# Performance work log

Hardware: AMD Instinct MI355X
Metric: run time of the kernel (lower is better)

## Reference

```python
import jax, jax.numpy as jnp
import numpy as np

B, S, D = 4, 2048, 1024
NH, NKV = 16, 4
DK = D // NH          # 64
NG = NH // NKV        # 4


def _rope_tables(seq, d_k):
    theta = 1.0 / jnp.power(10000.0, jnp.arange(0, d_k, 2, dtype=jnp.float32) / d_k)
    ang = jnp.outer(jnp.arange(seq, dtype=jnp.float32), theta)  # [S, DK/2]
    ang = jnp.concatenate([ang, ang], axis=-1)                   # [S, DK]
    return jnp.cos(ang), jnp.sin(ang)


def _rotate_half(t):
    half = t.shape[-1] // 2
    return jnp.concatenate([-t[..., half:], t[..., :half]], axis=-1)


def _apply_rope(t, cos, sin):
    # t: [B, H, S, DK]; cos/sin: [S, DK]
    return t * cos + _rotate_half(t) * sin


def setup_inputs() -> dict:
    key = jax.random.key(0)
    ks = jax.random.split(key, 5)
    sc = 0.02
    x = jax.random.normal(ks[0], (B, S, D), dtype=jnp.float32)
    Wq = jax.random.normal(ks[1], (D, NH * DK), dtype=jnp.float32) * sc
    Wk = jax.random.normal(ks[2], (D, NKV * DK), dtype=jnp.float32) * sc
    Wv = jax.random.normal(ks[3], (D, NKV * DK), dtype=jnp.float32) * sc
    Wo = jax.random.normal(ks[4], (D, D), dtype=jnp.float32) * sc
    mask = jnp.tril(jnp.ones((S, S), dtype=bool))[None, None]  # causal [1,1,S,S]
    return {"x": x, "Wq": Wq, "Wk": Wk, "Wv": Wv, "Wo": Wo, "mask": mask}


def reference(x, Wq, Wk, Wv, Wo, mask):
    batch, seq, _ = x.shape
    q = (x @ Wq).reshape(batch, seq, NH, DK).transpose(0, 2, 1, 3)    # [B,NH,S,DK]
    k = (x @ Wk).reshape(batch, seq, NKV, DK).transpose(0, 2, 1, 3)   # [B,NKV,S,DK]
    v = (x @ Wv).reshape(batch, seq, NKV, DK).transpose(0, 2, 1, 3)

    cos, sin = _rope_tables(seq, DK)
    q = _apply_rope(q, cos, sin)
    k = _apply_rope(k, cos, sin)

    # GQA: repeat_interleave K/V along head dim
    k = jnp.repeat(k, NG, axis=1)  # [B,NH,S,DK]
    v = jnp.repeat(v, NG, axis=1)

    scores = jnp.einsum('bhqd,bhkd->bhqk', q, k) / jnp.sqrt(jnp.float32(DK))
    scores = jnp.where(mask, scores, jnp.float32(-jnp.inf))
    weights = jax.nn.softmax(scores, axis=-1)
    out = jnp.einsum('bhqk,bhkd->bhqd', weights, v)          # [B,NH,S,DK]
    out = out.transpose(0, 2, 1, 3).reshape(batch, seq, D)   # [B,S,D]
    return out @ Wo
```

## Files before the change

### kernel.cpp

```cpp
#include <hip/hip_runtime.h>

#define DEV __device__ __forceinline__

typedef short s16x8 __attribute__((ext_vector_type(8)));
typedef float f32x4 __attribute__((ext_vector_type(4)));


DEV unsigned short f2bf(float f) {
  union { float f; unsigned int u; } a; a.f = f;
  unsigned int u = a.u;
  u = (u + 0x7FFFu + ((u >> 16) & 1u)) >> 16;
  return (unsigned short)u;
}

DEV unsigned int bfpack2(float a, float b) {
  union { float f; unsigned int u; } x, y; x.f = a; y.f = b;
  return ((x.u + 0x8000u) >> 16) | ((y.u + 0x8000u) & 0xFFFF0000u);
}

DEV unsigned int pktrunc(float a, float b) {
  union { float f; unsigned int u; } x, y; x.f = a; y.f = b;
  return __builtin_amdgcn_perm(y.u, x.u, 0x07060302u);
}

DEV void gl_lds16(const void* g, void* l) {
  __builtin_amdgcn_global_load_lds(
      (const __attribute__((address_space(1))) unsigned int*)g,
      (__attribute__((address_space(3))) unsigned int*)l, 16, 0, 0);
}

__global__ __launch_bounds__(256) void cvt_kern(const float* __restrict__ src,
                                                unsigned short* __restrict__ dst) {
  int i = blockIdx.x * 256 + threadIdx.x;
  float4 v = ((const float4*)src)[i];
  ushort4 o = make_ushort4(f2bf(v.x), f2bf(v.y), f2bf(v.z), f2bf(v.w));
  ((ushort4*)dst)[i] = o;
}

__global__ __launch_bounds__(256) void transp_kern(const float* __restrict__ src,
                                                   unsigned short* __restrict__ dst,
                                                   int src_cols, int dst_off) {
  __shared__ float tile[32][33];
  int k0 = blockIdx.x * 32, n0 = blockIdx.y * 32;
  int tx = threadIdx.x & 31, ty = threadIdx.x >> 5;
  #pragma unroll
  for (int i = ty; i < 32; i += 8)
    tile[i][tx] = src[(k0 + i) * src_cols + (n0 + tx)];
  __syncthreads();
  #pragma unroll
  for (int i = ty; i < 32; i += 8)
    dst[(size_t)(n0 + i + dst_off) * 1024 + (k0 + tx)] = f2bf(tile[tx][i]);
}

__global__ __launch_bounds__(256) void transp_qkv(const float* __restrict__ Wq,
                                                  const float* __restrict__ Wk,
                                                  const float* __restrict__ Wv,
                                                  unsigned short* __restrict__ dst) {
  __shared__ float tile[32][33];
  int k0 = blockIdx.x * 32, n0 = blockIdx.y * 32;
  const float* src; int sc, nloc;
  if (n0 < 1024)      { src = Wq; sc = 1024; nloc = n0; }
  else if (n0 < 1280) { src = Wk; sc = 256;  nloc = n0 - 1024; }
  else                { src = Wv; sc = 256;  nloc = n0 - 1280; }
  int tx = threadIdx.x & 31, ty = threadIdx.x >> 5;
  #pragma unroll
  for (int i = ty; i < 32; i += 8)
    tile[i][tx] = src[(k0 + i) * sc + (nloc + tx)];
  __syncthreads();
  #pragma unroll
  for (int i = ty; i < 32; i += 8)
    dst[(size_t)(n0 + i) * 1024 + (k0 + tx)] = f2bf(tile[tx][i]);
}

template <int EPI>
__global__ __launch_bounds__(256) void gemm128(
    const unsigned short* __restrict__ A,
    const unsigned short* __restrict__ BT,
    unsigned short* __restrict__ Qbuf,
    unsigned short* __restrict__ Kbuf,
    unsigned short* __restrict__ VTbuf,
    float* __restrict__ Cout) {
  __shared__ __align__(16) unsigned short As[128 * 64];
  __shared__ __align__(16) unsigned short Bs[128 * 64];
  const int K = 1024;
  int m0 = blockIdx.x * 128, n0 = blockIdx.y * 128;
  int tid = threadIdx.x, w = tid >> 6, lane = tid & 63;
  int c4 = lane & 15, quad = lane >> 4;
  int x7 = c4 & 7;
  int m_off = (w & 1) * 64, n_off = (w >> 1) * 64;

  f32x4 acc[4][4];
  #pragma unroll
  for (int i = 0; i < 4; i++)
    #pragma unroll
    for (int j = 0; j < 4; j++) acc[i][j] = (f32x4){0.f, 0.f, 0.f, 0.f};

  const unsigned short* pA[4];
  const unsigned short* pB[4];
  #pragma unroll
  for (int i = 0; i < 4; ++i) {
    int slot = i * 256 + tid;
    int row = slot >> 3, cs = slot & 7, lc = cs ^ (row & 7);
    pA[i] = A + (size_t)(m0 + row) * K + lc * 8;
    pB[i] = BT + (size_t)(n0 + row) * K + lc * 8;
  }

  for (int kt = 0; kt < K / 64; ++kt) {
    __syncthreads();
    #pragma unroll
    for (int i = 0; i < 4; ++i) {
      int slot = i * 256 + tid;
      gl_lds16(pA[i], (char*)As + slot * 16);
      gl_lds16(pB[i], (char*)Bs + slot * 16);
      pA[i] += 64; pB[i] += 64;
    }
    __syncthreads();
    #pragma unroll
    for (int kk = 0; kk < 2; ++kk) {
      s16x8 a[4], b[4];
      int cc = ((kk * 4 + quad) ^ x7) * 16;
      #pragma unroll
      for (int mi = 0; mi < 4; ++mi)
        a[mi] = *(const s16x8*)((const char*)As + (m_off + mi * 16 + c4) * 128 + cc);
      #pragma unroll
      for (int ni = 0; ni < 4; ++ni)
        b[ni] = *(const s16x8*)((const char*)Bs + (n_off + ni * 16 + c4) * 128 + cc);
      #pragma unroll
      for (int mi = 0; mi < 4; ++mi)
        #pragma unroll
        for (int ni = 0; ni < 4; ++ni)
          acc[mi][ni] = __builtin_amdgcn_mfma_f32_16x16x32_bf16(a[mi], b[ni], acc[mi][ni], 0, 0, 0);
    }
  }

  if (EPI == 1) {
    #pragma unroll
    for (int mi = 0; mi < 4; ++mi)
      #pragma unroll
      for (int ni = 0; ni < 4; ++ni)
        #pragma unroll
        for (int r = 0; r < 4; ++r) {
          int row = m0 + m_off + mi * 16 + quad * 4 + r;
          int col = n0 + n_off + ni * 16 + c4;
          Cout[(size_t)row * 1024 + col] = acc[mi][ni][r];
        }
  } else {
    int colbase = n0 + n_off;
    if (colbase < 1280) {
      const float CTH = 0.41524101186092029f;
      const float SC = 0.18033688011112042f;
      float th0 = exp2f(-(float)c4 * CTH);
      float th1 = exp2f(-(float)(c4 + 16) * CTH);
      bool isQ = colbase < 1024;
      float osc = isQ ? SC : 1.0f;
      #pragma unroll
      for (int mi = 0; mi < 4; ++mi)
        #pragma unroll
        for (int r = 0; r < 4; ++r) {
          int row = m0 + m_off + mi * 16 + quad * 4 + r;
          float pos = (float)(row & 2047);
          float a0 = pos * th0, a1 = pos * th1;
          float c0 = __cosf(a0), s0 = __sinf(a0);
          float c1 = __cosf(a1), s1 = __sinf(a1);
          float v0 = acc[mi][0][r], v1 = acc[mi][1][r];
          float v2 = acc[mi][2][r], v3 = acc[mi][3][r];
          float o0 = (v0 * c0 - v2 * s0) * osc;
          float o1 = (v1 * c1 - v3 * s1) * osc;
          float o2 = (v2 * c0 + v0 * s0) * osc;
          float o3 = (v3 * c1 + v1 * s1) * osc;
          if (isQ) {
            size_t base = (size_t)row * 1024 + colbase + c4;
            Qbuf[base] = f2bf(o0); Qbuf[base + 16] = f2bf(o1);
            Qbuf[base + 32] = f2bf(o2); Qbuf[base + 48] = f2bf(o3);
          } else {
            size_t base = (size_t)row * 256 + (colbase - 1024) + c4;
            Kbuf[base] = f2bf(o0); Kbuf[base + 16] = f2bf(o1);
            Kbuf[base + 32] = f2bf(o2); Kbuf[base + 48] = f2bf(o3);
          }
        }
    } else {
      #pragma unroll
      for (int mi = 0; mi < 4; ++mi)
        #pragma unroll
        for (int ni = 0; ni < 4; ++ni) {
          int row = m0 + m_off + mi * 16 + quad * 4;
          int c = colbase + ni * 16 + c4 - 1280;
          int bb = row >> 11, s = row & 2047;
          uint2 pv = make_uint2(bfpack2(acc[mi][ni][0], acc[mi][ni][1]),
                                bfpack2(acc[mi][ni][2], acc[mi][ni][3]));
          *(uint2*)(VTbuf + ((size_t)(bb * 256 + c)) * 2048 + s) = pv;
        }
    }
  }
}

__global__ __launch_bounds__(128, 2) void attn_kern(
    const unsigned short* __restrict__ Qbuf,
    const unsigned short* __restrict__ Kbuf,
    const unsigned short* __restrict__ VTbuf,
    unsigned short* __restrict__ Obuf) {
  __shared__ __align__(16) unsigned short Ks[2][64 * 64];
  __shared__ __align__(16) unsigned short VTs[2][64 * 64];
  __shared__ __align__(16) unsigned short Ps[2 * 32 * 64];

  int pr = blockIdx.x;
  int h = blockIdx.y, b = blockIdx.z, g = h >> 2;
  int tid = threadIdx.x, w = tid >> 6, lane = tid & 63;
  int c4 = lane & 15, quad = lane >> 4;
  int x7 = c4 & 7;
  unsigned short* Pw = Ps + w * 2048;

  const unsigned short* kB[4];
  const unsigned short* vB[4];
  #pragma unroll
  for (int i = 0; i < 4; ++i) {
    int L = i * 128 + tid;
    int row = L >> 3, cs = (L & 7) ^ (row & 7);
    kB[i] = Kbuf + (size_t)(b * 2048 + row) * 256 + g * 64 + cs * 8;
    vB[i] = VTbuf + (size_t)(b * 256 + g * 64 + row) * 2048 + cs * 8;
  }

  for (int ph = 0; ph < 2; ++ph) {
    int qtile = ph ? (31 - pr) : pr;
    int nkv = qtile + 1;
    int q0 = qtile * 64;

    s16x8 bq[2][2];
    #pragma unroll
    for (int gg = 0; gg < 2; ++gg)
      #pragma unroll
      for (int kk = 0; kk < 2; ++kk)
        bq[gg][kk] = *(const s16x8*)(Qbuf +
            (size_t)(b * 2048 + q0 + w * 32 + gg * 16 + c4) * 1024 +
            h * 64 + kk * 32 + quad * 8);

    const unsigned short* kS[4];
    const unsigned short* vS[4];
    #pragma unroll
    for (int i = 0; i < 4; ++i) { kS[i] = kB[i]; vS[i] = vB[i]; }

    f32x4 Oacc[2][4];
    float lacc[2] = {0.f, 0.f};
    #pragma unroll
    for (int gg = 0; gg < 2; ++gg)
      #pragma unroll
      for (int nd = 0; nd < 4; ++nd) Oacc[gg][nd] = (f32x4){0.f, 0.f, 0.f, 0.f};

    __syncthreads();
    #pragma unroll
    for (int i = 0; i < 4; ++i) {
      int L = i * 128 + tid;
      gl_lds16(kS[i], (char*)Ks[0] + L * 16);
      gl_lds16(vS[i], (char*)VTs[0] + L * 16);
      kS[i] += 64 * 256; vS[i] += 64;
    }

    for (int kt = 0; kt < nkv; ++kt) {
      int cur = kt & 1, nxt = cur ^ 1;
      __syncthreads();

      if (kt + 1 < nkv) {
        #pragma unroll
        for (int i = 0; i < 4; ++i) {
          int L = i * 128 + tid;
          gl_lds16(kS[i], (char*)Ks[nxt] + L * 16);
          gl_lds16(vS[i], (char*)VTs[nxt] + L * 16);
          kS[i] += 64 * 256; vS[i] += 64;
        }
      }

      const char* Kc = (const char*)Ks[cur];
      const char* Vc = (const char*)VTs[cur];

      f32x4 st[2][4];
      #pragma unroll
      for (int gg = 0; gg < 2; ++gg)
        #pragma unroll
        for (int mt = 0; mt < 4; ++mt) st[gg][mt] = (f32x4){0.f, 0.f, 0.f, 0.f};
      #pragma unroll
      for (int kk = 0; kk < 2; ++kk) {
        #pragma unroll
        for (int mt = 0; mt < 4; ++mt) {
          s16x8 ak = *(const s16x8*)(Kc + (mt * 16 + c4) * 128 +
                                     ((kk * 4 + quad) ^ x7) * 16);
          st[0][mt] = __builtin_amdgcn_mfma_f32_16x16x32_bf16(ak, bq[0][kk], st[0][mt], 0, 0, 0);
          st[1][mt] = __builtin_amdgcn_mfma_f32_16x16x32_bf16(ak, bq[1][kk], st[1][mt], 0, 0, 0);
        }
      }

      #pragma unroll
      for (int gg = 0; gg < 2; ++gg) {
        int qmin = q0 + w * 32 + gg * 16;
        if (kt * 64 + 63 > qmin) {
          int qi = qmin + c4;
          #pragma unroll
          for (int mt = 0; mt < 4; ++mt)
            #pragma unroll
            for (int r = 0; r < 4; ++r) {
              int kv = kt * 64 + mt * 16 + quad * 4 + r;
              if (kv > qi) st[gg][mt][r] = -1e30f;
            }
        }
        int rr = gg * 16 + c4;
        #pragma unroll
        for (int mt = 0; mt < 4; ++mt) {
          float e0 = exp2f(st[gg][mt][0]);
          float e1 = exp2f(st[gg][mt][1]);
          float e2 = exp2f(st[gg][mt][2]);
          float e3 = exp2f(st[gg][mt][3]);
          lacc[gg] += (e0 + e1) + (e2 + e3);
          unsigned int lo = pktrunc(e0, e1);
          unsigned int hi = pktrunc(e2, e3);
          int cc = (mt * 2 + (quad >> 1)) ^ x7;
          *(uint2*)((char*)Pw + rr * 128 + cc * 16 + (quad & 1) * 8) =
              make_uint2(lo, hi);
        }
      }

      #pragma unroll
      for (int kk = 0; kk < 2; ++kk) {
        s16x8 ap0 = *(const s16x8*)((const char*)Pw + c4 * 128 +
                                    ((kk * 4 + quad) ^ x7) * 16);
        s16x8 ap1 = *(const s16x8*)((const char*)Pw + (16 + c4) * 128 +
                                    ((kk * 4 + quad) ^ x7) * 16);
        #pragma unroll
        for (int nd = 0; nd < 4; ++nd) {
          s16x8 av = *(const s16x8*)(Vc + (nd * 16 + c4) * 128 +
                                     ((kk * 4 + quad) ^ x7) * 16);
          Oacc[0][nd] = __builtin_amdgcn_mfma_f32_16x16x32_bf16(av, ap0, Oacc[0][nd], 0, 0, 0);
          Oacc[1][nd] = __builtin_amdgcn_mfma_f32_16x16x32_bf16(av, ap1, Oacc[1][nd], 0, 0, 0);
        }
      }
    }

    #pragma unroll
    for (int gg = 0; gg < 2; ++gg) {
      float ls = lacc[gg];
      ls += __shfl_xor(ls, 16);
      ls += __shfl_xor(ls, 32);
      float linv = 1.f / ls;
      int rr = gg * 16 + c4;
      #pragma unroll
      for (int nd = 0; nd < 4; ++nd) {
        unsigned int lo = bfpack2(Oacc[gg][nd][0] * linv, Oacc[gg][nd][1] * linv);
        unsigned int hi = bfpack2(Oacc[gg][nd][2] * linv, Oacc[gg][nd][3] * linv);
        int cc = (nd * 2 + (quad >> 1)) ^ x7;
        *(uint2*)((char*)Pw + rr * 128 + cc * 16 + (quad & 1) * 8) =
            make_uint2(lo, hi);
      }
    }
    {
      int row = lane >> 1;
      int grow = b * 2048 + q0 + w * 32 + row;
      #pragma unroll
      for (int j = 0; j < 4; ++j) {
        int cb = (lane & 1) * 4 + j;
        uint4 v = *(const uint4*)((const char*)Pw + row * 128 +
                                  (cb ^ (row & 7)) * 16);
        *(uint4*)(Obuf + (size_t)grow * 1024 + h * 64 + cb * 8) = v;
      }
    }
  }
}

extern "C" void kernel_launch(void* const* d_in, const int* in_sizes, int n_in,
                              void* d_out, int out_size, void* d_ws, size_t ws_size,
                              hipStream_t stream) {
  const float* x  = (const float*)d_in[0];
  const float* Wq = (const float*)d_in[1];
  const float* Wk = (const float*)d_in[2];
  const float* Wv = (const float*)d_in[3];
  const float* Wo = (const float*)d_in[4];
  float* out = (float*)d_out;

  unsigned short* xb    = (unsigned short*)d_ws;
  unsigned short* WqkvT = xb + 8192 * 1024;
  unsigned short* WoT   = WqkvT + 1536 * 1024;
  unsigned short* Qbuf  = WoT + 1024 * 1024;
  unsigned short* Kbuf  = Qbuf + 8192 * 1024;
  unsigned short* VTbuf = Kbuf + 8192 * 256;
  unsigned short* Obuf  = VTbuf + 4 * 256 * 2048;

  cvt_kern<<<8192, 256, 0, stream>>>(x, xb);
  transp_qkv<<<dim3(32, 48), 256, 0, stream>>>(Wq, Wk, Wv, WqkvT);
  transp_kern<<<dim3(32, 32), 256, 0, stream>>>(Wo, WoT, 1024, 0);

  gemm128<0><<<dim3(64, 12), 256, 0, stream>>>(xb, WqkvT, Qbuf, Kbuf, VTbuf, nullptr);
  attn_kern<<<dim3(16, 16, 4), 128, 0, stream>>>(Qbuf, Kbuf, VTbuf, Obuf);
  gemm128<1><<<dim3(64, 8), 256, 0, stream>>>(Obuf, WoT, nullptr, nullptr, nullptr, out);
}
```

Baseline: 243.1 us.

## Double-buffer GEMM LDS tiles with K=32 stages and merge weight transposes

```diff
diff --git a/kernel.cpp b/kernel.cpp
--- a/kernel.cpp
+++ b/kernel.cpp
@@ -37,31 +37,20 @@
   ((ushort4*)dst)[i] = o;
 }
 
-__global__ __launch_bounds__(256) void transp_kern(const float* __restrict__ src,
-                                                   unsigned short* __restrict__ dst,
-                                                   int src_cols, int dst_off) {
+__global__ __launch_bounds__(256) void transp_all(const float* __restrict__ Wq,
+                                                  const float* __restrict__ Wk,
+                                                  const float* __restrict__ Wv,
+                                                  const float* __restrict__ Wo,
+                                                  unsigned short* __restrict__ WqkvT,
+                                                  unsigned short* __restrict__ WoT) {
   __shared__ float tile[32][33];
   int k0 = blockIdx.x * 32, n0 = blockIdx.y * 32;
-  int tx = threadIdx.x & 31, ty = threadIdx.x >> 5;
-  #pragma unroll
-  for (int i = ty; i < 32; i += 8)
-    tile[i][tx] = src[(k0 + i) * src_cols + (n0 + tx)];
-  __syncthreads();
-  #pragma unroll
-  for (int i = ty; i < 32; i += 8)
-    dst[(size_t)(n0 + i + dst_off) * 1024 + (k0 + tx)] = f2bf(tile[tx][i]);
-}
-
-__global__ __launch_bounds__(256) void transp_qkv(const float* __restrict__ Wq,
-                                                  const float* __restrict__ Wk,
-                                                  const float* __restrict__ Wv,
-                                                  unsigned short* __restrict__ dst) {
-  __shared__ float tile[32][33];
-  int k0 = blockIdx.x * 32, n0 = blockIdx.y * 32;
-  const float* src; int sc, nloc;
-  if (n0 < 1024)      { src = Wq; sc = 1024; nloc = n0; }
-  else if (n0 < 1280) { src = Wk; sc = 256;  nloc = n0 - 1024; }
-  else                { src = Wv; sc = 256;  nloc = n0 - 1280; }
+  const float* src; int sc, nloc, drow;
+  unsigned short* dst;
+  if (n0 < 1024)      { src = Wq; sc = 1024; nloc = n0;        dst = WqkvT; drow = n0; }
+  else if (n0 < 1280) { src = Wk; sc = 256;  nloc = n0 - 1024; dst = WqkvT; drow = n0; }
+  else if (n0 < 1536) { src = Wv; sc = 256;  nloc = n0 - 1280; dst = WqkvT; drow = n0; }
+  else                { src = Wo; sc = 1024; nloc = n0 - 1536; dst = WoT;   drow = n0 - 1536; }
   int tx = threadIdx.x & 31, ty = threadIdx.x >> 5;
   #pragma unroll
   for (int i = ty; i < 32; i += 8)
@@ -69,24 +58,25 @@
   __syncthreads();
   #pragma unroll
   for (int i = ty; i < 32; i += 8)
-    dst[(size_t)(n0 + i) * 1024 + (k0 + tx)] = f2bf(tile[tx][i]);
+    dst[(size_t)(drow + i) * 1024 + (k0 + tx)] = f2bf(tile[tx][i]);
 }
 
 template <int EPI>
-__global__ __launch_bounds__(256) void gemm128(
+__global__ __launch_bounds__(256, 4) void gemm128(
     const unsigned short* __restrict__ A,
     const unsigned short* __restrict__ BT,
     unsigned short* __restrict__ Qbuf,
     unsigned short* __restrict__ Kbuf,
     unsigned short* __restrict__ VTbuf,
     float* __restrict__ Cout) {
-  __shared__ __align__(16) unsigned short As[128 * 64];
-  __shared__ __align__(16) unsigned short Bs[128 * 64];
+  __shared__ __align__(16) unsigned short As[2][128 * 32];
+  __shared__ __align__(16) unsigned short Bs[2][128 * 32];
   const int K = 1024;
+  const int NKT = K / 32;
   int m0 = blockIdx.x * 128, n0 = blockIdx.y * 128;
   int tid = threadIdx.x, w = tid >> 6, lane = tid & 63;
   int c4 = lane & 15, quad = lane >> 4;
-  int x7 = c4 & 7;
+  int x3 = c4 & 3;
   int m_off = (w & 1) * 64, n_off = (w >> 1) * 64;
 
   f32x4 acc[4][4];
@@ -95,42 +85,51 @@
     #pragma unroll
     for (int j = 0; j < 4; j++) acc[i][j] = (f32x4){0.f, 0.f, 0.f, 0.f};
 
-  const unsigned short* pA[4];
-  const unsigned short* pB[4];
-  #pragma unroll
-  for (int i = 0; i < 4; ++i) {
+  const unsigned short* pA[2];
+  const unsigned short* pB[2];
+  #pragma unroll
+  for (int i = 0; i < 2; ++i) {
     int slot = i * 256 + tid;
-    int row = slot >> 3, cs = slot & 7, lc = cs ^ (row & 7);
+    int row = slot >> 2, cs = slot & 3, lc = cs ^ (row & 3);
     pA[i] = A + (size_t)(m0 + row) * K + lc * 8;
     pB[i] = BT + (size_t)(n0 + row) * K + lc * 8;
   }
 
-  for (int kt = 0; kt < K / 64; ++kt) {
+  #pragma unroll
+  for (int i = 0; i < 2; ++i) {
+    int slot = i * 256 + tid;
+    gl_lds16(pA[i], (char*)As[0] + slot * 16);
+    gl_lds16(pB[i], (char*)Bs[0] + slot * 16);
+    pA[i] += 32; pB[i] += 32;
+  }
+
+  int cc = (quad ^ x3) * 16;
+  for (int kt = 0; kt < NKT; ++kt) {
+    int cur = kt & 1, nxt = cur ^ 1;
     __syncthreads();
-    #pragma unroll
-    for (int i = 0; i < 4; ++i) {
-      int slot = i * 256 + tid;
-      gl_lds16(pA[i], (char*)As + slot * 16);
-      gl_lds16(pB[i], (char*)Bs + slot * 16);
-      pA[i] += 64; pB[i] += 64;
-    }
-    __syncthreads();
-    #pragma unroll
-    for (int kk = 0; kk < 2; ++kk) {
-      s16x8 a[4], b[4];
-      int cc = ((kk * 4 + quad) ^ x7) * 16;
-      #pragma unroll
-      for (int mi = 0; mi < 4; ++mi)
-        a[mi] = *(const s16x8*)((const char*)As + (m_off + mi * 16 + c4) * 128 + cc);
+
+    if (kt + 1 < NKT) {
+      #pragma unroll
+      for (int i = 0; i < 2; ++i) {
+        int slot = i * 256 + tid;
+        gl_lds16(pA[i], (char*)As[nxt] + slot * 16);
+        gl_lds16(pB[i], (char*)Bs[nxt] + slot * 16);
+        pA[i] += 32; pB[i] += 32;
+      }
+    }
+
+    s16x8 a[4], b[4];
+    #pragma unroll
+    for (int mi = 0; mi < 4; ++mi)
+      a[mi] = *(const s16x8*)((const char*)As[cur] + (m_off + mi * 16 + c4) * 64 + cc);
+    #pragma unroll
+    for (int ni = 0; ni < 4; ++ni)
+      b[ni] = *(const s16x8*)((const char*)Bs[cur] + (n_off + ni * 16 + c4) * 64 + cc);
+    #pragma unroll
+    for (int mi = 0; mi < 4; ++mi)
       #pragma unroll
       for (int ni = 0; ni < 4; ++ni)
-        b[ni] = *(const s16x8*)((const char*)Bs + (n_off + ni * 16 + c4) * 128 + cc);
-      #pragma unroll
-      for (int mi = 0; mi < 4; ++mi)
-        #pragma unroll
-        for (int ni = 0; ni < 4; ++ni)
-          acc[mi][ni] = __builtin_amdgcn_mfma_f32_16x16x32_bf16(a[mi], b[ni], acc[mi][ni], 0, 0, 0);
-    }
+        acc[mi][ni] = __builtin_amdgcn_mfma_f32_16x16x32_bf16(a[mi], b[ni], acc[mi][ni], 0, 0, 0);
   }
 
   if (EPI == 1) {
@@ -382,8 +381,7 @@
   unsigned short* Obuf  = VTbuf + 4 * 256 * 2048;
 
   cvt_kern<<<8192, 256, 0, stream>>>(x, xb);
-  transp_qkv<<<dim3(32, 48), 256, 0, stream>>>(Wq, Wk, Wv, WqkvT);
-  transp_kern<<<dim3(32, 32), 256, 0, stream>>>(Wo, WoT, 1024, 0);
+  transp_all<<<dim3(32, 80), 256, 0, stream>>>(Wq, Wk, Wv, Wo, WqkvT, WoT);
 
   gemm128<0><<<dim3(64, 12), 256, 0, stream>>>(xb, WqkvT, Qbuf, Kbuf, VTbuf, nullptr);
   attn_kern<<<dim3(16, 16, 4), 128, 0, stream>>>(Qbuf, Kbuf, VTbuf, Obuf);
```

After: 239.6 us. Within noise of the previous version (-1.4%).
